# Kernel optimization log

Measured on AMD Instinct MI355X. Metric: run time of the kernel, lower is better.

Reference implementation:

```python
import jax, jax.numpy as jnp
import numpy as np

K, N, M, D = 64, 8192, 8, 32  # locations, time steps, covariate features, memory depth


def setup_inputs() -> dict:
    key = jax.random.key(0)
    ks = jax.random.split(key, 6)
    obs = jax.random.uniform(ks[0], (K, N), dtype=jnp.float32)            # event counts [K, N]
    covs = jax.random.normal(ks[1], (K, N, M), dtype=jnp.float32)          # covariates  [K, N, M]
    hbeta = jnp.array([2.0], dtype=jnp.float32)                            # decay rate param (torch init: 2)
    halpha = jax.random.uniform(ks[2], (K, K), dtype=jnp.float32) * 0.01   # excitation matrix, U(0, 0.01)
    gamma = jax.random.uniform(ks[3], (K,), dtype=jnp.float32) * 0.01      # covariate gate, U(0, 0.01)
    W1 = jax.random.normal(ks[4], (20, 2 * D * M), dtype=jnp.float32) * 0.05
    b1 = jnp.zeros((20,), dtype=jnp.float32)
    W2 = jax.random.normal(ks[5], (1, 20), dtype=jnp.float32) * 0.05
    b2 = jnp.zeros((1,), dtype=jnp.float32)
    return dict(obs=obs, covs=covs, hbeta=hbeta, halpha=halpha, gamma=gamma,
                W1=W1, b1=b1, W2=W2, b2=b2)


def _forward(obs, covs, hbeta, halpha, gamma, W1, b1, W2, b2):
    k, n = obs.shape
    beta = hbeta[0]
    decay = jnp.exp(-beta)

    # Excitation: S[t] = sum_{tp < t} obs[:, tp] * beta * exp(-(t - tp) * beta)
    # exact O(N) linear recurrence instead of the original per-t O(t) resummation.
    def step(S, o):
        return decay * (S + beta * o), S
    _, S_all = jax.lax.scan(step, jnp.zeros((k,), obs.dtype), obs.T)  # [N, K]
    lam1 = jax.nn.softplus(jnp.einsum('kj,nj->kn', halpha, S_all))     # [K, N] (hmu = 0 in subclass)

    # Edge-padded covariate windows: window at t is padded[:, t : t + 2D, :]
    padded = jnp.concatenate([
        jnp.repeat(covs[:, :1, :], D, axis=1),   # left pad with first step
        covs,
        jnp.repeat(covs[:, -1:, :], D, axis=1),  # right pad with last step
    ], axis=1)                                   # [K, N + 2D, M]
    idx = jnp.arange(n)[:, None] + jnp.arange(2 * D)[None, :]  # [N, 2D]
    X = padded[:, idx, :].reshape(k, n, 2 * D * M)             # [K, N, 2DM], time-major then M (matches torch reshape)

    # Tiny 2-layer MLP with softplus activations, vectorized over (K, N)
    h = jax.nn.softplus(jnp.einsum('knf,hf->knh', X, W1) + b1)           # [K, N, 20]
    mu = jax.nn.softplus(jnp.einsum('knh,oh->kno', h, W2) + b2)[..., 0]  # [K, N]

    lams = lam1 + gamma[:, None] * mu                                    # [K, N]
    loglik = jnp.sum(obs * jnp.log(lams) - lams)
    return loglik, lams


def reference(obs, covs, hbeta, halpha, gamma, W1, b1, W2, b2):
    return _forward(obs, covs, hbeta, halpha, gamma, W1, b1, W2, b2)
```

## Files before the change

### kernel.cpp

```cpp
#include <hip/hip_runtime.h>
#include <hip/hip_bf16.h>
#include <math.h>

#define KL 64
#define NT 8192
#define MF 8
#define DD 32
#define WIN 64
#define HD 20
#define HP 32
#define KF 512
#define NB 256
#define NXB (NT / NB)
#define NBLK (NXB * KL)
#define NPART (NBLK * 4)
#define BPSZ (64 * 32 * 8)

typedef __attribute__((ext_vector_type(8))) short bf16x8;
typedef __attribute__((ext_vector_type(4))) float f32x4;
typedef __attribute__((ext_vector_type(4))) unsigned u32x4;

__device__ __forceinline__ float softplus_f(float x) {
    float e = __expf(-fabsf(x));
    return fmaxf(x, 0.0f) + __logf(1.0f + e);
}
__device__ __forceinline__ short f2bf(float x) {
    __hip_bfloat16 h = __float2bfloat16(x);
    return *reinterpret_cast<short*>(&h);
}
__device__ __forceinline__ unsigned pkbf(float a, float b) {
    unsigned r;
    asm("v_cvt_pk_bf16_f32 %0, %1, %2" : "=v"(r) : "v"(a), "v"(b));
    return r;
}

__global__ __launch_bounds__(256)
void pack_kernel(const float* __restrict__ W1, const float* __restrict__ b1,
                 const float* __restrict__ W2, const float* __restrict__ hbeta,
                 short* __restrict__ Bp, float* __restrict__ b1p,
                 float* __restrict__ W2p, float* __restrict__ wtab) {
    int t = blockIdx.x * 256 + threadIdx.x;
    #pragma unroll
    for (int i = 0; i < 4; ++i) {
        int p = t + i * 4096;
        int m = p & 7;
        int dc = p >> 3;
        int h = dc & 31;
        int d = dc >> 5;
        Bp[p] = (h < HD) ? f2bf(W1[h * KF + d * 8 + m]) : (short)0;
    }
    if (blockIdx.x == 0 && threadIdx.x < HP) {
        b1p[threadIdx.x] = (threadIdx.x < HD) ? b1[threadIdx.x] : 0.0f;
        W2p[threadIdx.x] = (threadIdx.x < HD) ? W2[threadIdx.x] : 0.0f;
    }
    if (blockIdx.x == 0 && threadIdx.x < WIN) {
        float bt = hbeta[0];
        wtab[threadIdx.x] = bt * __expf(-bt * (float)(threadIdx.x + 1));
    }
}

__global__ __launch_bounds__(256)
void mlp_mfma_kernel(const float* __restrict__ covs, const float* __restrict__ obs,
                     const float* __restrict__ halpha, const float* __restrict__ hbeta,
                     const short* __restrict__ Bp, const float* __restrict__ b1p,
                     const float* __restrict__ W2p, const float* __restrict__ b2,
                     const float* __restrict__ gamma, const float* __restrict__ wt,
                     float* __restrict__ lams, float* __restrict__ partial) {
    __shared__ short cov_s[4][128 * MF];
    __shared__ float T_s[4][128];

    int k    = blockIdx.y;
    int n0   = blockIdx.x * NB;
    int tid  = threadIdx.x;
    int lane = tid & 63;
    int wave = tid >> 6;
    int base = n0 + wave * 64;
    int c    = lane & 15;
    int g    = lane >> 4;

    int n = base + lane;
    size_t idx = (size_t)k * NT + n;
    float obs_n = obs[idx];
    float beta  = hbeta[0];
    float gam   = gamma[k];
    float b2v   = b2[0];
    float4 w2lo = *(const float4*)&W2p[g * 4];
    float4 w2hi = *(const float4*)&W2p[16 + g * 4];
    float4 b1lo = *(const float4*)&b1p[g * 4];
    float4 b1hi = *(const float4*)&b1p[16 + g * 4];

    const float* cbase = covs + (size_t)k * NT * MF;
    {
        int t1 = base - DD + lane;
        t1 = t1 < 0 ? 0 : t1;
        int t2 = base + DD + lane;
        t2 = t2 > NT - 1 ? NT - 1 : t2;
        const float4* cp1 = (const float4*)(cbase + (size_t)t1 * MF);
        const float4* cp2 = (const float4*)(cbase + (size_t)t2 * MF);
        float4 a0 = cp1[0], a1 = cp1[1];
        float4 d0 = cp2[0], d1 = cp2[1];
        u32x4 q1 = { pkbf(a0.x, a0.y), pkbf(a0.z, a0.w),
                     pkbf(a1.x, a1.y), pkbf(a1.z, a1.w) };
        u32x4 q2 = { pkbf(d0.x, d0.y), pkbf(d0.z, d0.w),
                     pkbf(d1.x, d1.y), pkbf(d1.z, d1.w) };
        *(u32x4*)&cov_s[wave][lane * MF] = q1;
        *(u32x4*)&cov_s[wave][(lane + 64) * MF] = q2;
    }

    f32x4 acc[4][2];
    #pragma unroll
    for (int mt = 0; mt < 4; ++mt) {
        acc[mt][0] = (f32x4){0.f, 0.f, 0.f, 0.f};
        acc[mt][1] = (f32x4){0.f, 0.f, 0.f, 0.f};
    }

    const short* pAw = Bp + g * 256 + c * 8;
    const short* pBc = &cov_s[wave][(c + g) * MF];

    const float* arow = halpha + (size_t)k * KL;
    int tA = base - WIN + lane;
    tA = tA < 0 ? 0 : tA;
    int tB = base + lane;
    float aA = 0.0f, aB = 0.0f;

    #pragma unroll 2
    for (int kk = 0; kk < KF / 32; ++kk) {
        #pragma unroll
        for (int jj = 0; jj < 4; ++jj) {
            int j = kk * 4 + jj;
            float ajv = arow[j];
            const float* orow = obs + (size_t)j * NT;
            aA = fmaf(ajv, orow[tA], aA);
            aB = fmaf(ajv, orow[tB], aB);
        }
        bf16x8 aw0 = *(const bf16x8*)(pAw + kk * 1024);
        bf16x8 aw1 = *(const bf16x8*)(pAw + kk * 1024 + 128);
        #pragma unroll
        for (int mt = 0; mt < 4; ++mt) {
            bf16x8 bc = *(const bf16x8*)(pBc + (mt * 16 + kk * 4) * MF);
            acc[mt][0] = __builtin_amdgcn_mfma_f32_16x16x32_bf16(aw0, bc, acc[mt][0], 0, 0, 0);
            acc[mt][1] = __builtin_amdgcn_mfma_f32_16x16x32_bf16(aw1, bc, acc[mt][1], 0, 0, 0);
        }
    }
    T_s[wave][lane] = aA;
    T_s[wave][64 + lane] = aB;

    float pre = 0.0f;
    #pragma unroll
    for (int mt = 0; mt < 4; ++mt) {
        float p = 0.0f;
        #pragma unroll
        for (int r = 0; r < 4; ++r) {
            p = fmaf(((const float*)&w2lo)[r],
                     softplus_f(acc[mt][0][r] + ((const float*)&b1lo)[r]), p);
            p = fmaf(((const float*)&w2hi)[r],
                     softplus_f(acc[mt][1][r] + ((const float*)&b1hi)[r]), p);
        }
        p += __shfl_xor(p, 16, 64);
        p += __shfl_xor(p, 32, 64);
        pre = (g == mt) ? p : pre;
    }

    const float* Tp = &T_s[wave][64 + lane];
    float la = 0.0f;
    if (base >= WIN && beta >= 1.6667f) {
        float la0 = 0.f, la1 = 0.f, la2 = 0.f, la3 = 0.f;
        #pragma unroll
        for (int it = 0; it < 5; ++it) {
            la0 = fmaf(wt[4 * it + 0], Tp[-(4 * it + 1)], la0);
            la1 = fmaf(wt[4 * it + 1], Tp[-(4 * it + 2)], la1);
            la2 = fmaf(wt[4 * it + 2], Tp[-(4 * it + 3)], la2);
            la3 = fmaf(wt[4 * it + 3], Tp[-(4 * it + 4)], la3);
        }
        la = (la0 + la1) + (la2 + la3);
    } else {
        float decay = __expf(-beta);
        int Lmax = (int)(30.0f / beta) + 2;
        if (Lmax > WIN) Lmax = WIN;
        float w = beta * decay;
        for (int i = 1; i <= Lmax; ++i) {
            if (i <= n) la = fmaf(w, Tp[-i], la);
            w *= decay;
        }
    }
    float lam1 = softplus_f(la);
    float mu = softplus_f(pre + b2v);
    float lam = lam1 + gam * mu;
    lams[idx] = lam;
    float term = fmaf(obs_n, __logf(lam), -lam);

    #pragma unroll
    for (int off = 32; off > 0; off >>= 1) term += __shfl_down(term, off, 64);
    if (lane == 0)
        partial[((size_t)blockIdx.y * NXB + blockIdx.x) * 4 + wave] = term;
}

__global__ __launch_bounds__(256)
void finalize_kernel(const float* __restrict__ partial, float* __restrict__ out0) {
    __shared__ float wred[4];
    int tid = threadIdx.x;
    float s = 0.0f;
    #pragma unroll
    for (int i = 0; i < NPART / 256; ++i) s += partial[i * 256 + tid];
    #pragma unroll
    for (int off = 32; off > 0; off >>= 1) s += __shfl_down(s, off, 64);
    if ((tid & 63) == 0) wred[tid >> 6] = s;
    __syncthreads();
    if (tid == 0) out0[0] = (wred[0] + wred[1]) + (wred[2] + wred[3]);
}

extern "C" void kernel_launch(void* const* d_in, const int* in_sizes, int n_in,
                              void* d_out, int out_size, void* d_ws, size_t ws_size,
                              hipStream_t stream) {
    const float* obs    = (const float*)d_in[0];
    const float* covs   = (const float*)d_in[1];
    const float* hbeta  = (const float*)d_in[2];
    const float* halpha = (const float*)d_in[3];
    const float* gamma  = (const float*)d_in[4];
    const float* W1     = (const float*)d_in[5];
    const float* b1     = (const float*)d_in[6];
    const float* W2     = (const float*)d_in[7];
    const float* b2     = (const float*)d_in[8];

    float* out  = (float*)d_out;
    float* lams = out + 1;

    char* ws = (char*)d_ws;
    float* partial = (float*)ws;
    float* b1p     = (float*)(ws + 32768);
    float* W2p     = (float*)(ws + 32896);
    float* wtab    = (float*)(ws + 33024);
    short* Bp      = (short*)(ws + 33280);

    pack_kernel<<<dim3(16), dim3(256), 0, stream>>>(W1, b1, W2, hbeta,
                                                    Bp, b1p, W2p, wtab);
    mlp_mfma_kernel<<<dim3(NXB, KL), dim3(256), 0, stream>>>(
        covs, obs, halpha, hbeta, Bp, b1p, W2p, b2, gamma, wtab, lams, partial);
    finalize_kernel<<<1, dim3(256), 0, stream>>>(partial, out);
}
```

Measured before the change: 41.70 us.

## Process 256 time steps per wave to amortize halo and window overheads

Each wave now handles 256 time steps instead of 64, with blocks covering 1024 steps. The 64-row halo loads for covariates and for the excitation history are shared across four output chunks, and the W1 fragments loaded per k-step feed 16 MFMA tiles instead of 4. The cost is many more accumulator registers (128 floats for acc) and a grid four times smaller (512 blocks), which may lower occupancy and latency hiding.

```diff
diff --git a/kernel.cpp b/kernel.cpp
--- a/kernel.cpp
+++ b/kernel.cpp
@@ -10,7 +10,7 @@
 #define HD 20
 #define HP 32
 #define KF 512
-#define NB 256
+#define NB 1024
 #define NXB (NT / NB)
 #define NBLK (NXB * KL)
 #define NPART (NBLK * 4)
@@ -66,88 +66,94 @@
                      const float* __restrict__ W2p, const float* __restrict__ b2,
                      const float* __restrict__ gamma, const float* __restrict__ wt,
                      float* __restrict__ lams, float* __restrict__ partial) {
-    __shared__ short cov_s[4][128 * MF];
-    __shared__ float T_s[4][128];
+    __shared__ short cov_s[4][320 * MF];
+    __shared__ float T_s[4][320];
 
     int k    = blockIdx.y;
     int n0   = blockIdx.x * NB;
     int tid  = threadIdx.x;
     int lane = tid & 63;
     int wave = tid >> 6;
-    int base = n0 + wave * 64;
+    int base = n0 + wave * 256;
     int c    = lane & 15;
     int g    = lane >> 4;
 
     int n = base + lane;
     size_t idx = (size_t)k * NT + n;
-    float obs_n = obs[idx];
+    float obs_n0 = obs[idx];
+    float obs_n1 = obs[idx + 64];
+    float obs_n2 = obs[idx + 128];
+    float obs_n3 = obs[idx + 192];
     float beta  = hbeta[0];
     float gam   = gamma[k];
     float b2v   = b2[0];
+
+    const float* cbase = covs + (size_t)k * NT * MF;
+    #pragma unroll
+    for (int s = 0; s < 5; ++s) {
+        int tt = base - DD + s * 64 + lane;
+        tt = tt < 0 ? 0 : (tt > NT - 1 ? NT - 1 : tt);
+        const float4* cp = (const float4*)(cbase + (size_t)tt * MF);
+        float4 a0 = cp[0], a1 = cp[1];
+        u32x4 q = { pkbf(a0.x, a0.y), pkbf(a0.z, a0.w),
+                    pkbf(a1.x, a1.y), pkbf(a1.z, a1.w) };
+        *(u32x4*)&cov_s[wave][(s * 64 + lane) * MF] = q;
+    }
+
+    f32x4 acc[16][2];
+    #pragma unroll
+    for (int mt = 0; mt < 16; ++mt) {
+        acc[mt][0] = (f32x4){0.f, 0.f, 0.f, 0.f};
+        acc[mt][1] = (f32x4){0.f, 0.f, 0.f, 0.f};
+    }
+
+    const short* pAw = Bp + g * 256 + c * 8;
+    const short* pBc = &cov_s[wave][(c + g) * MF];
+
+    const float* arow = halpha + (size_t)k * KL;
+    int i0 = base - WIN + lane;
+    i0 = i0 < 0 ? 0 : i0;
+    int i1 = base + lane;
+    int i2 = base + 64 + lane;
+    int i3 = base + 128 + lane;
+    int i4 = base + 192 + lane;
+    float aT0 = 0.f, aT1 = 0.f, aT2 = 0.f, aT3 = 0.f, aT4 = 0.f;
+
+    #pragma unroll 2
+    for (int kk = 0; kk < KF / 32; ++kk) {
+        #pragma unroll
+        for (int jj = 0; jj < 4; ++jj) {
+            int j = kk * 4 + jj;
+            float ajv = arow[j];
+            const float* orow = obs + (size_t)j * NT;
+            aT0 = fmaf(ajv, orow[i0], aT0);
+            aT1 = fmaf(ajv, orow[i1], aT1);
+            aT2 = fmaf(ajv, orow[i2], aT2);
+            aT3 = fmaf(ajv, orow[i3], aT3);
+            aT4 = fmaf(ajv, orow[i4], aT4);
+        }
+        bf16x8 aw0 = *(const bf16x8*)(pAw + kk * 1024);
+        bf16x8 aw1 = *(const bf16x8*)(pAw + kk * 1024 + 128);
+        #pragma unroll
+        for (int mt = 0; mt < 16; ++mt) {
+            bf16x8 bc = *(const bf16x8*)(pBc + (mt * 16 + kk * 4) * MF);
+            acc[mt][0] = __builtin_amdgcn_mfma_f32_16x16x32_bf16(aw0, bc, acc[mt][0], 0, 0, 0);
+            acc[mt][1] = __builtin_amdgcn_mfma_f32_16x16x32_bf16(aw1, bc, acc[mt][1], 0, 0, 0);
+        }
+    }
+    T_s[wave][lane] = aT0;
+    T_s[wave][64 + lane] = aT1;
+    T_s[wave][128 + lane] = aT2;
+    T_s[wave][192 + lane] = aT3;
+    T_s[wave][256 + lane] = aT4;
+
     float4 w2lo = *(const float4*)&W2p[g * 4];
     float4 w2hi = *(const float4*)&W2p[16 + g * 4];
     float4 b1lo = *(const float4*)&b1p[g * 4];
     float4 b1hi = *(const float4*)&b1p[16 + g * 4];
-
-    const float* cbase = covs + (size_t)k * NT * MF;
-    {
-        int t1 = base - DD + lane;
-        t1 = t1 < 0 ? 0 : t1;
-        int t2 = base + DD + lane;
-        t2 = t2 > NT - 1 ? NT - 1 : t2;
-        const float4* cp1 = (const float4*)(cbase + (size_t)t1 * MF);
-        const float4* cp2 = (const float4*)(cbase + (size_t)t2 * MF);
-        float4 a0 = cp1[0], a1 = cp1[1];
-        float4 d0 = cp2[0], d1 = cp2[1];
-        u32x4 q1 = { pkbf(a0.x, a0.y), pkbf(a0.z, a0.w),
-                     pkbf(a1.x, a1.y), pkbf(a1.z, a1.w) };
-        u32x4 q2 = { pkbf(d0.x, d0.y), pkbf(d0.z, d0.w),
-                     pkbf(d1.x, d1.y), pkbf(d1.z, d1.w) };
-        *(u32x4*)&cov_s[wave][lane * MF] = q1;
-        *(u32x4*)&cov_s[wave][(lane + 64) * MF] = q2;
-    }
-
-    f32x4 acc[4][2];
-    #pragma unroll
-    for (int mt = 0; mt < 4; ++mt) {
-        acc[mt][0] = (f32x4){0.f, 0.f, 0.f, 0.f};
-        acc[mt][1] = (f32x4){0.f, 0.f, 0.f, 0.f};
-    }
-
-    const short* pAw = Bp + g * 256 + c * 8;
-    const short* pBc = &cov_s[wave][(c + g) * MF];
-
-    const float* arow = halpha + (size_t)k * KL;
-    int tA = base - WIN + lane;
-    tA = tA < 0 ? 0 : tA;
-    int tB = base + lane;
-    float aA = 0.0f, aB = 0.0f;
-
-    #pragma unroll 2
-    for (int kk = 0; kk < KF / 32; ++kk) {
-        #pragma unroll
-        for (int jj = 0; jj < 4; ++jj) {
-            int j = kk * 4 + jj;
-            float ajv = arow[j];
-            const float* orow = obs + (size_t)j * NT;
-            aA = fmaf(ajv, orow[tA], aA);
-            aB = fmaf(ajv, orow[tB], aB);
-        }
-        bf16x8 aw0 = *(const bf16x8*)(pAw + kk * 1024);
-        bf16x8 aw1 = *(const bf16x8*)(pAw + kk * 1024 + 128);
-        #pragma unroll
-        for (int mt = 0; mt < 4; ++mt) {
-            bf16x8 bc = *(const bf16x8*)(pBc + (mt * 16 + kk * 4) * MF);
-            acc[mt][0] = __builtin_amdgcn_mfma_f32_16x16x32_bf16(aw0, bc, acc[mt][0], 0, 0, 0);
-            acc[mt][1] = __builtin_amdgcn_mfma_f32_16x16x32_bf16(aw1, bc, acc[mt][1], 0, 0, 0);
-        }
-    }
-    T_s[wave][lane] = aA;
-    T_s[wave][64 + lane] = aB;
-
-    float pre = 0.0f;
-    #pragma unroll
-    for (int mt = 0; mt < 4; ++mt) {
+    float pre0 = 0.f, pre1 = 0.f, pre2 = 0.f, pre3 = 0.f;
+    #pragma unroll
+    for (int mt = 0; mt < 16; ++mt) {
         float p = 0.0f;
         #pragma unroll
         for (int r = 0; r < 4; ++r) {
@@ -158,36 +164,55 @@
         }
         p += __shfl_xor(p, 16, 64);
         p += __shfl_xor(p, 32, 64);
-        pre = (g == mt) ? p : pre;
-    }
-
-    const float* Tp = &T_s[wave][64 + lane];
-    float la = 0.0f;
+        if (mt < 4)       pre0 = (g == mt)      ? p : pre0;
+        else if (mt < 8)  pre1 = (g == mt - 4)  ? p : pre1;
+        else if (mt < 12) pre2 = (g == mt - 8)  ? p : pre2;
+        else              pre3 = (g == mt - 12) ? p : pre3;
+    }
+
+    const float* Tq0 = &T_s[wave][64 + lane];
+    const float* Tq1 = &T_s[wave][128 + lane];
+    const float* Tq2 = &T_s[wave][192 + lane];
+    const float* Tq3 = &T_s[wave][256 + lane];
+    float la0 = 0.f, la1 = 0.f, la2 = 0.f, la3 = 0.f;
     if (base >= WIN && beta >= 1.6667f) {
-        float la0 = 0.f, la1 = 0.f, la2 = 0.f, la3 = 0.f;
         #pragma unroll
         for (int it = 0; it < 5; ++it) {
-            la0 = fmaf(wt[4 * it + 0], Tp[-(4 * it + 1)], la0);
-            la1 = fmaf(wt[4 * it + 1], Tp[-(4 * it + 2)], la1);
-            la2 = fmaf(wt[4 * it + 2], Tp[-(4 * it + 3)], la2);
-            la3 = fmaf(wt[4 * it + 3], Tp[-(4 * it + 4)], la3);
-        }
-        la = (la0 + la1) + (la2 + la3);
+            #pragma unroll
+            for (int u = 0; u < 4; ++u) {
+                float w = wt[4 * it + u];
+                int off = 4 * it + u + 1;
+                la0 = fmaf(w, Tq0[-off], la0);
+                la1 = fmaf(w, Tq1[-off], la1);
+                la2 = fmaf(w, Tq2[-off], la2);
+                la3 = fmaf(w, Tq3[-off], la3);
+            }
+        }
     } else {
         float decay = __expf(-beta);
         int Lmax = (int)(30.0f / beta) + 2;
         if (Lmax > WIN) Lmax = WIN;
         float w = beta * decay;
         for (int i = 1; i <= Lmax; ++i) {
-            if (i <= n) la = fmaf(w, Tp[-i], la);
+            if (i <= n)       la0 = fmaf(w, Tq0[-i], la0);
+            if (i <= n + 64)  la1 = fmaf(w, Tq1[-i], la1);
+            if (i <= n + 128) la2 = fmaf(w, Tq2[-i], la2);
+            if (i <= n + 192) la3 = fmaf(w, Tq3[-i], la3);
             w *= decay;
         }
     }
-    float lam1 = softplus_f(la);
-    float mu = softplus_f(pre + b2v);
-    float lam = lam1 + gam * mu;
-    lams[idx] = lam;
-    float term = fmaf(obs_n, __logf(lam), -lam);
+    float lamA = softplus_f(la0) + gam * softplus_f(pre0 + b2v);
+    float lamB = softplus_f(la1) + gam * softplus_f(pre1 + b2v);
+    float lamC = softplus_f(la2) + gam * softplus_f(pre2 + b2v);
+    float lamD = softplus_f(la3) + gam * softplus_f(pre3 + b2v);
+    lams[idx]       = lamA;
+    lams[idx + 64]  = lamB;
+    lams[idx + 128] = lamC;
+    lams[idx + 192] = lamD;
+    float term = fmaf(obs_n0, __logf(lamA), -lamA)
+               + fmaf(obs_n1, __logf(lamB), -lamB)
+               + fmaf(obs_n2, __logf(lamC), -lamC)
+               + fmaf(obs_n3, __logf(lamD), -lamD);
 
     #pragma unroll
     for (int off = 32; off > 0; off >>= 1) term += __shfl_down(term, off, 64);
```

After: 55.89 us. 34.0% more time.
